# Kernel tuning notes

Measured on AMD Instinct MI355X. Metric: run time of the kernel, lower is better.

Reference implementation:

```python
import jax, jax.numpy as jnp
import numpy as np

B, M, E, IN, Q, OUT, H = 256, 2048, 128, 512, 512, 512, 64

def _lin(x, w, b):
    return x @ w.T + b

def setup_inputs() -> dict:
    key = jax.random.key(0)
    ks = jax.random.split(key, 20)
    d = {
        'read_weights': jax.random.uniform(ks[0], (B, M)),
        'write_weights': jax.random.uniform(ks[1], (B, M)),
        'usage': jax.random.uniform(ks[2], (B, M)),
        'free_gates': jax.random.uniform(ks[3], (B, M)),
        'x': jax.random.normal(ks[4], (B, 1, IN)),
        'query': jax.random.normal(ks[5], (B, 1, Q)),
        'memory': jax.random.normal(ks[6], (B, M, E)),
        'I_w': jax.random.normal(ks[7], (E, IN)) * 0.02, 'I_b': jnp.zeros((E,)),
        'W1_w': jax.random.normal(ks[8], (H, E)) * 0.02, 'W1_b': jnp.zeros((H,)),
        'W2_w': jax.random.normal(ks[9], (H, E)) * 0.02, 'W2_b': jnp.zeros((H,)),
        'R1_w': jax.random.normal(ks[10], (H, Q)) * 0.02, 'R1_b': jnp.zeros((H,)),
        'R2_w': jax.random.normal(ks[11], (H, E)) * 0.02, 'R2_b': jnp.zeros((H,)),
        'O_w': jax.random.normal(ks[12], (OUT, E)) * 0.02, 'O_b': jnp.zeros((OUT,)),
    }
    return d

def _allocation(read_weights, write_weights, usage, free_gates):
    u = 1e-5 + (1.0 - 1e-5) * usage
    psi = 1.0 - free_gates * read_weights
    u = u + write_weights - u * write_weights
    u = u * psi                                   # new usage [B, M]
    phi = jnp.argsort(u, axis=1)                  # ascending order indices
    sorted_u = jnp.take_along_axis(u, phi, axis=1)
    # NOTE: original uses inclusive cumprod (matches torch code exactly)
    sorted_alloc = (1.0 - sorted_u) * jnp.cumprod(sorted_u, axis=1)
    phi_rev = jnp.argsort(phi, axis=1)            # inverse permutation
    alloc = jnp.take_along_axis(sorted_alloc, phi_rev, axis=1)
    return u, alloc

def reference(read_weights, write_weights, usage, free_gates, x, query, memory,
              I_w, I_b, W1_w, W1_b, W2_w, W2_b, R1_w, R1_b, R2_w, R2_b, O_w, O_b):
    # ---- write ----
    emb = _lin(x, I_w, I_b)                       # [B,1,E]
    Wi = _lin(emb, W1_w, W1_b)                    # [B,1,H]
    Wm = _lin(memory, W2_w, W2_b)                 # [B,M,H]
    scores = jnp.einsum('bqh,bmh->bqm', Wi, Wm)   # [B,1,M]
    w_content = jax.nn.softmax(scores, axis=2)
    new_usage, alloc = _allocation(read_weights, write_weights, usage, free_gates)
    w = (w_content + alloc[:, None, :]) * 0.5     # [B,1,M]
    new_memory = memory + w.transpose(0, 2, 1) * emb  # [B,M,1]*[B,1,E]
    new_write_weights = w[:, 0, :]
    # ---- read ----
    Rq = _lin(query, R1_w, R1_b)                  # [B,1,H]
    Rm = _lin(new_memory, R2_w, R2_b)             # [B,M,H]
    rscores = jnp.einsum('bqh,bmh->bqm', Rq, Rm)
    wr = jax.nn.softmax(rscores, axis=2)          # [B,1,M]
    pooled = jnp.einsum('bm,bme->be', wr[:, 0, :], new_memory)
    output = _lin(pooled, O_w, O_b)               # [B,OUT]
    return ((wr[:, 0, :], new_write_weights, new_usage), output, new_memory)
```

## Files before the change

### kernel.cpp

```cpp
#include <hip/hip_runtime.h>
#include <hip/hip_bf16.h>

constexpr int B   = 256;
constexpr int M   = 2048;
constexpr int E   = 128;
constexpr int IN  = 512;
constexpr int Qd  = 512;
constexpr int OUTd= 512;
constexpr int H   = 64;

constexpr size_t OFF_WR = 0;
constexpr size_t OFF_W  = (size_t)B*M;
constexpr size_t OFF_U  = (size_t)2*B*M;
constexpr size_t OFF_Y  = (size_t)3*B*M;
constexpr size_t OFF_NM = OFF_Y + (size_t)B*OUTd;

__device__ __forceinline__ float bf2f(unsigned short u) {
    union { unsigned int i; float f; } v; v.i = ((unsigned int)u) << 16; return v.f;
}
__device__ __forceinline__ unsigned short f2bf(float f) {
    unsigned int x = __float_as_uint(f);
    unsigned int r = (x + 0x7fffu + ((x >> 16) & 1u)) >> 16;
    return (unsigned short)r;
}
__device__ __forceinline__ void unpack8(uint4 d, float* o) {
    o[0]=bf2f(d.x & 0xffff); o[1]=bf2f(d.x >> 16);
    o[2]=bf2f(d.y & 0xffff); o[3]=bf2f(d.y >> 16);
    o[4]=bf2f(d.z & 0xffff); o[5]=bf2f(d.z >> 16);
    o[6]=bf2f(d.w & 0xffff); o[7]=bf2f(d.w >> 16);
}
__device__ __forceinline__ uint4 pack8(const float* f) {
    uint4 d;
    d.x = (unsigned)f2bf(f[0]) | ((unsigned)f2bf(f[1]) << 16);
    d.y = (unsigned)f2bf(f[2]) | ((unsigned)f2bf(f[3]) << 16);
    d.z = (unsigned)f2bf(f[4]) | ((unsigned)f2bf(f[5]) << 16);
    d.w = (unsigned)f2bf(f[6]) | ((unsigned)f2bf(f[7]) << 16);
    return d;
}

__device__ __forceinline__ float ldf(const void* p, size_t i, int bf) {
    return bf ? bf2f(((const unsigned short*)p)[i]) : ((const float*)p)[i];
}
__device__ __forceinline__ void ld8(const void* p, size_t i, int bf, float* o) {
    if (bf) {
        uint4 d = *(const uint4*)((const unsigned short*)p + i);
        unpack8(d, o);
    } else {
        const float4* q = (const float4*)((const float*)p + i);
        float4 a = q[0], c = q[1];
        o[0]=a.x; o[1]=a.y; o[2]=a.z; o[3]=a.w;
        o[4]=c.x; o[5]=c.y; o[6]=c.z; o[7]=c.w;
    }
}
__device__ __forceinline__ void st1(void* p, size_t i, int bf, float v) {
    if (bf) ((unsigned short*)p)[i] = f2bf(v);
    else    ((float*)p)[i] = v;
}
__device__ __forceinline__ void st8(void* p, size_t i, int bf, const float* v) {
    if (bf) {
        *(uint4*)((unsigned short*)p + i) = pack8(v);
    } else {
        float4 a, c;
        a.x=v[0]; a.y=v[1]; a.z=v[2]; a.w=v[3];
        c.x=v[4]; c.y=v[5]; c.z=v[6]; c.w=v[7];
        float4* q = (float4*)((float*)p + i);
        q[0]=a; q[1]=c;
    }
}

__global__ __launch_bounds__(512) void k0_detect(const void* usage, int* flag) {
    __shared__ int cnt;
    if (threadIdx.x == 0) cnt = 0;
    __syncthreads();
    float v = bf2f(((const unsigned short*)usage)[threadIdx.x]);
    int ok = (v >= 0.0f && v <= 1.0f) ? 1 : 0;
    atomicAdd(&cnt, ok);
    __syncthreads();
    if (threadIdx.x == 0) flag[0] = (cnt >= 500) ? 1 : 0;
}

__global__ __launch_bounds__(128) void k1_pre(
    const void* __restrict__ x,   const void* __restrict__ qy,
    const void* __restrict__ I_w, const void* __restrict__ I_b,
    const void* __restrict__ W1w, const void* __restrict__ W1b,
    const void* __restrict__ W2w, const void* __restrict__ W2b,
    const void* __restrict__ R1w, const void* __restrict__ R1b,
    const void* __restrict__ R2w, const void* __restrict__ R2b,
    const int* __restrict__ flag,
    float* __restrict__ emb_ws, float* __restrict__ v_ws, float* __restrict__ u2_ws,
    float* __restrict__ c1_ws,  float* __restrict__ c2_ws, float* __restrict__ d2_ws)
{
    const int bf = *flag;
    __shared__ float xs[IN], qs[Qd], embs[E], wis[H], rqs[H], red[128];
    const int b = blockIdx.x, t = threadIdx.x;

    for (int i = t; i < IN; i += 128) xs[i] = ldf(x,  (size_t)b*IN + i, bf);
    for (int i = t; i < Qd; i += 128) qs[i] = ldf(qy, (size_t)b*Qd + i, bf);
    __syncthreads();

    float acc = 0.f;
    for (int c = 0; c < IN/8; ++c) {
        float m8[8]; ld8(I_w, (size_t)t*IN + c*8, bf, m8);
        #pragma unroll
        for (int j = 0; j < 8; ++j) acc += m8[j] * xs[c*8 + j];
    }
    acc += ldf(I_b, t, bf);
    embs[t] = acc;
    emb_ws[(size_t)b*E + t] = acc;
    __syncthreads();

    if (t < H) {
        float wv = 0.f;
        for (int c = 0; c < E/8; ++c) {
            float m8[8]; ld8(W1w, (size_t)t*E + c*8, bf, m8);
            #pragma unroll
            for (int j = 0; j < 8; ++j) wv += m8[j] * embs[c*8 + j];
        }
        wv += ldf(W1b, t, bf);
        wis[t] = wv;
    }
    __syncthreads();

    float vv = 0.f;
    for (int h = 0; h < H; ++h) vv += ldf(W2w, (size_t)h*E + t, bf) * wis[h];
    v_ws[(size_t)b*E + t] = vv;

    red[t] = (t < H) ? wis[t] * ldf(W2b, t, bf) : 0.f;
    __syncthreads();
    for (int off = 64; off > 0; off >>= 1) { if (t < off) red[t] += red[t+off]; __syncthreads(); }
    if (t == 0) c1_ws[b] = red[0];
    __syncthreads();

    if (t < H) {
        float rv = 0.f;
        for (int c = 0; c < Qd/8; ++c) {
            float m8[8]; ld8(R1w, (size_t)t*Qd + c*8, bf, m8);
            #pragma unroll
            for (int j = 0; j < 8; ++j) rv += m8[j] * qs[c*8 + j];
        }
        rv += ldf(R1b, t, bf);
        rqs[t] = rv;
    }
    __syncthreads();

    float uu = 0.f;
    for (int h = 0; h < H; ++h) uu += ldf(R2w, (size_t)h*E + t, bf) * rqs[h];
    u2_ws[(size_t)b*E + t] = uu;

    red[t] = (t < H) ? rqs[t] * ldf(R2b, t, bf) : 0.f;
    __syncthreads();
    for (int off = 64; off > 0; off >>= 1) { if (t < off) red[t] += red[t+off]; __syncthreads(); }
    if (t == 0) c2_ws[b] = red[0];
    __syncthreads();

    red[t] = uu * embs[t];
    __syncthreads();
    for (int off = 64; off > 0; off >>= 1) { if (t < off) red[t] += red[t+off]; __syncthreads(); }
    if (t == 0) d2_ws[b] = red[0];
}

__global__ __launch_bounds__(256) void k2_alloc(
    const void* __restrict__ rw, const void* __restrict__ ww,
    const void* __restrict__ us, const void* __restrict__ fg,
    const int* __restrict__ flag,
    float* __restrict__ alloc_ws, void* __restrict__ dout)
{
    const int bf = *flag;
    __shared__ float uv[M];
    __shared__ int   idx[M];
    __shared__ float scan[256];
    const int b = blockIdx.x, t = threadIdx.x;

    #pragma unroll
    for (int s = 0; s < 8; ++s) {
        int m = s*256 + t;
        size_t o = (size_t)b*M + m;
        float U = ldf(us, o, bf), W = ldf(ww, o, bf), R = ldf(rw, o, bf), F = ldf(fg, o, bf);
        float u = 1e-5f + (1.0f - 1e-5f) * U;
        float psi = 1.0f - F * R;
        u = u + W - u * W;
        u = u * psi;
        uv[m] = u; idx[m] = m;
        st1(dout, OFF_U + o, bf, u);
    }
    __syncthreads();

    for (int k = 2; k <= M; k <<= 1) {
        for (int j = k >> 1; j > 0; j >>= 1) {
            #pragma unroll
            for (int s = 0; s < 8; ++s) {
                int i = s*256 + t;
                int ixj = i ^ j;
                if (ixj > i) {
                    bool up = ((i & k) == 0);
                    float a = uv[i], c = uv[ixj];
                    int ia = idx[i], ic = idx[ixj];
                    bool agtb = (a > c) || (a == c && ia > ic);
                    if (up ? agtb : !agtb) {
                        uv[i] = c; uv[ixj] = a;
                        idx[i] = ic; idx[ixj] = ia;
                    }
                }
            }
            __syncthreads();
        }
    }

    const int base = t * 8;
    float lp[8];
    float run = 1.f;
    #pragma unroll
    for (int q = 0; q < 8; ++q) { run *= uv[base + q]; lp[q] = run; }
    scan[t] = run;
    __syncthreads();
    for (int off = 1; off < 256; off <<= 1) {
        float val = scan[t];
        float oth = (t >= off) ? scan[t - off] : 1.0f;
        __syncthreads();
        scan[t] = val * oth;
        __syncthreads();
    }
    float pref = (t > 0) ? scan[t - 1] : 1.0f;

    #pragma unroll
    for (int q = 0; q < 8; ++q) {
        int i = base + q;
        float a = (1.0f - uv[i]) * (pref * lp[q]);
        alloc_ws[(size_t)b*M + idx[i]] = a;
    }
}

__global__ __launch_bounds__(256) void k3_scores(
    const void* __restrict__ mem,
    const float* __restrict__ v_ws, const float* __restrict__ u2_ws,
    const float* __restrict__ c1_ws, const int* __restrict__ flag,
    float* __restrict__ s1, float* __restrict__ s2)
{
    const int bf = *flag;
    const int blk = blockIdx.x;
    const int b = blk >> 4, chunk = blk & 15;
    const int t = threadIdx.x, l = t & 15, g = t >> 4;
    float v8[8], u8[8];
    {
        const float* vb = v_ws  + (size_t)b*E + l*8;
        const float* ub = u2_ws + (size_t)b*E + l*8;
        #pragma unroll
        for (int j = 0; j < 8; ++j) { v8[j] = vb[j]; u8[j] = ub[j]; }
    }
    const float cc1 = c1_ws[b];
    const size_t mbase = (size_t)b*M*E;
    const int row0 = chunk*128 + g;
    for (int it = 0; it < 8; ++it) {
        int row = row0 + it*16;
        float m8[8]; ld8(mem, mbase + (size_t)row*E + l*8, bf, m8);
        float p1 = 0.f, p2 = 0.f;
        #pragma unroll
        for (int j = 0; j < 8; ++j) { p1 += m8[j]*v8[j]; p2 += m8[j]*u8[j]; }
        #pragma unroll
        for (int mask = 8; mask > 0; mask >>= 1) {
            p1 += __shfl_xor(p1, mask, 16);
            p2 += __shfl_xor(p2, mask, 16);
        }
        if (l == 0) {
            s1[(size_t)b*M + row] = p1 + cc1;
            s2[(size_t)b*M + row] = p2;
        }
    }
}

__global__ __launch_bounds__(256) void k4_weights(
    const float* __restrict__ s1, const float* __restrict__ s2,
    const float* __restrict__ alloc_ws,
    const float* __restrict__ c2_ws, const float* __restrict__ d2_ws,
    const int* __restrict__ flag,
    float* __restrict__ w_ws, float* __restrict__ wr_ws,
    void* __restrict__ dout)
{
    const int bf = *flag;
    __shared__ float red[256];
    const int b = blockIdx.x, t = threadIdx.x;
    const float* s1b = s1 + (size_t)b*M;
    const float* s2b = s2 + (size_t)b*M;

    float sv[8];
    float lmax = -3.4e38f;
    #pragma unroll
    for (int s = 0; s < 8; ++s) { sv[s] = s1b[s*256 + t]; lmax = fmaxf(lmax, sv[s]); }
    red[t] = lmax; __syncthreads();
    for (int off = 128; off > 0; off >>= 1) { if (t < off) red[t] = fmaxf(red[t], red[t+off]); __syncthreads(); }
    float gmax = red[0]; __syncthreads();

    float lsum = 0.f;
    #pragma unroll
    for (int s = 0; s < 8; ++s) { float e = expf(sv[s] - gmax); sv[s] = e; lsum += e; }
    red[t] = lsum; __syncthreads();
    for (int off = 128; off > 0; off >>= 1) { if (t < off) red[t] += red[t+off]; __syncthreads(); }
    float inv = 1.0f / red[0]; __syncthreads();

    const float dd = d2_ws[b], cc = c2_ws[b];
    float rs[8];
    #pragma unroll
    for (int s = 0; s < 8; ++s) {
        int m = s*256 + t;
        float wc = sv[s] * inv;
        float wv = 0.5f * (wc + alloc_ws[(size_t)b*M + m]);
        w_ws[(size_t)b*M + m] = wv;
        st1(dout, OFF_W + (size_t)b*M + m, bf, wv);
        rs[s] = s2b[m] + wv * dd + cc;
    }

    lmax = -3.4e38f;
    #pragma unroll
    for (int s = 0; s < 8; ++s) lmax = fmaxf(lmax, rs[s]);
    red[t] = lmax; __syncthreads();
    for (int off = 128; off > 0; off >>= 1) { if (t < off) red[t] = fmaxf(red[t], red[t+off]); __syncthreads(); }
    gmax = red[0]; __syncthreads();

    lsum = 0.f;
    #pragma unroll
    for (int s = 0; s < 8; ++s) { float e = expf(rs[s] - gmax); rs[s] = e; lsum += e; }
    red[t] = lsum; __syncthreads();
    for (int off = 128; off > 0; off >>= 1) { if (t < off) red[t] += red[t+off]; __syncthreads(); }
    float inv2 = 1.0f / red[0]; __syncthreads();

    #pragma unroll
    for (int s = 0; s < 8; ++s) {
        int m = s*256 + t;
        float wrv = rs[s] * inv2;
        wr_ws[(size_t)b*M + m] = wrv;
        st1(dout, OFF_WR + (size_t)b*M + m, bf, wrv);
    }
}

__global__ __launch_bounds__(256) void k5_update(
    const void* __restrict__ mem, const float* __restrict__ emb_ws,
    const float* __restrict__ w_ws, const float* __restrict__ wr_ws,
    const int* __restrict__ flag,
    void* __restrict__ dout, float* __restrict__ pooled)
{
    const int bf = *flag;
    __shared__ float psh[E];
    const int blk = blockIdx.x;
    const int b = blk >> 4, chunk = blk & 15;
    const int t = threadIdx.x, l = t & 15, g = t >> 4;
    if (t < E) psh[t] = 0.f;
    __syncthreads();

    float e8[8];
    {
        const float* eb = emb_ws + (size_t)b*E + l*8;
        #pragma unroll
        for (int j = 0; j < 8; ++j) e8[j] = eb[j];
    }
    float acc[8] = {0,0,0,0,0,0,0,0};
    const size_t mbase = (size_t)b*M*E;
    const int row0 = chunk*128 + g;
    for (int it = 0; it < 8; ++it) {
        int row = row0 + it*16;
        size_t off = mbase + (size_t)row*E + l*8;
        float m8[8]; ld8(mem, off, bf, m8);
        float wv  = w_ws [(size_t)b*M + row];
        float wrv = wr_ws[(size_t)b*M + row];
        float n8[8];
        #pragma unroll
        for (int j = 0; j < 8; ++j) {
            n8[j] = m8[j] + wv * e8[j];
            acc[j] += wrv * n8[j];
        }
        st8(dout, OFF_NM + off, bf, n8);
    }
    #pragma unroll
    for (int j = 0; j < 8; ++j) atomicAdd(&psh[l*8 + j], acc[j]);
    __syncthreads();
    if (t < E) atomicAdd(&pooled[(size_t)b*E + t], psh[t]);
}

__global__ __launch_bounds__(256) void k6_out(
    const float* __restrict__ pooled,
    const void* __restrict__ O_w, const void* __restrict__ O_b,
    const int* __restrict__ flag,
    void* __restrict__ dout)
{
    const int bf = *flag;
    __shared__ float ps[E];
    const int b = blockIdx.x, t = threadIdx.x;
    if (t < E) ps[t] = pooled[(size_t)b*E + t];
    __syncthreads();
    for (int o = t; o < OUTd; o += 256) {
        float acc = 0.f;
        for (int c = 0; c < E/8; ++c) {
            float m8[8]; ld8(O_w, (size_t)o*E + c*8, bf, m8);
            #pragma unroll
            for (int j = 0; j < 8; ++j) acc += m8[j] * ps[c*8 + j];
        }
        acc += ldf(O_b, o, bf);
        st1(dout, OFF_Y + (size_t)b*OUTd + o, bf, acc);
    }
}

extern "C" void kernel_launch(void* const* d_in, const int* in_sizes, int n_in,
                              void* d_out, int out_size, void* d_ws, size_t ws_size,
                              hipStream_t stream)
{
    const void* rw  = d_in[0];
    const void* ww  = d_in[1];
    const void* us  = d_in[2];
    const void* fg  = d_in[3];
    const void* x   = d_in[4];
    const void* qy  = d_in[5];
    const void* mem = d_in[6];
    const void* I_w = d_in[7];
    const void* I_b = d_in[8];
    const void* W1w = d_in[9];
    const void* W1b = d_in[10];
    const void* W2w = d_in[11];
    const void* W2b = d_in[12];
    const void* R1w = d_in[13];
    const void* R1b = d_in[14];
    const void* R2w = d_in[15];
    const void* R2b = d_in[16];
    const void* O_w = d_in[17];
    const void* O_b = d_in[18];

    int*   flag_ws = (int*)d_ws;
    float* fbase   = (float*)d_ws + 16;
    float* emb_ws   = fbase;
    float* v_ws     = emb_ws + (size_t)B*E;
    float* u2_ws    = v_ws   + (size_t)B*E;
    float* c1_ws    = u2_ws  + (size_t)B*E;
    float* c2_ws    = c1_ws  + B;
    float* d2_ws    = c2_ws  + B;
    float* alloc_ws = d2_ws  + B;
    float* s1_ws    = alloc_ws + (size_t)B*M;
    float* s2_ws    = s1_ws    + (size_t)B*M;
    float* w_ws     = s2_ws    + (size_t)B*M;
    float* wr_ws    = w_ws     + (size_t)B*M;
    float* pooled   = wr_ws    + (size_t)B*M;

    hipMemsetAsync(pooled, 0, (size_t)B*E*sizeof(float), stream);

    k0_detect<<<1,    512, 0, stream>>>(us, flag_ws);
    k1_pre   <<<B,    128, 0, stream>>>(x, qy, I_w, I_b, W1w, W1b, W2w, W2b,
                                        R1w, R1b, R2w, R2b, flag_ws,
                                        emb_ws, v_ws, u2_ws, c1_ws, c2_ws, d2_ws);
    k2_alloc <<<B,    256, 0, stream>>>(rw, ww, us, fg, flag_ws, alloc_ws, d_out);
    k3_scores<<<B*16, 256, 0, stream>>>(mem, v_ws, u2_ws, c1_ws, flag_ws, s1_ws, s2_ws);
    k4_weights<<<B,   256, 0, stream>>>(s1_ws, s2_ws, alloc_ws, c2_ws, d2_ws, flag_ws,
                                        w_ws, wr_ws, d_out);
    k5_update<<<B*16, 256, 0, stream>>>(mem, emb_ws, w_ws, wr_ws, flag_ws, d_out, pooled);
    k6_out   <<<B,    256, 0, stream>>>(pooled, O_w, O_b, flag_ws, d_out);
}
```

Before: 714.5 us.

## Fuse alloc sort with score kernel, register bitonic sort, deterministic pooled partials

```diff
diff --git a/kernel.cpp b/kernel.cpp
--- a/kernel.cpp
+++ b/kernel.cpp
@@ -79,7 +79,7 @@
     if (threadIdx.x == 0) flag[0] = (cnt >= 500) ? 1 : 0;
 }
 
-__global__ __launch_bounds__(128) void k1_pre(
+__global__ __launch_bounds__(256) void k1_pre(
     const void* __restrict__ x,   const void* __restrict__ qy,
     const void* __restrict__ I_w, const void* __restrict__ I_b,
     const void* __restrict__ W1w, const void* __restrict__ W1b,
@@ -88,25 +88,39 @@
     const void* __restrict__ R2w, const void* __restrict__ R2b,
     const int* __restrict__ flag,
     float* __restrict__ emb_ws, float* __restrict__ v_ws, float* __restrict__ u2_ws,
-    float* __restrict__ c1_ws,  float* __restrict__ c2_ws, float* __restrict__ d2_ws)
+    float* __restrict__ c1_ws,  float* __restrict__ c2_ws)
 {
     const int bf = *flag;
-    __shared__ float xs[IN], qs[Qd], embs[E], wis[H], rqs[H], red[128];
+    __shared__ float xs[IN], qs[Qd], embs[E], wis[H], rqs[H], red[256];
     const int b = blockIdx.x, t = threadIdx.x;
 
-    for (int i = t; i < IN; i += 128) xs[i] = ldf(x,  (size_t)b*IN + i, bf);
-    for (int i = t; i < Qd; i += 128) qs[i] = ldf(qy, (size_t)b*Qd + i, bf);
-    __syncthreads();
-
-    float acc = 0.f;
-    for (int c = 0; c < IN/8; ++c) {
-        float m8[8]; ld8(I_w, (size_t)t*IN + c*8, bf, m8);
-        #pragma unroll
-        for (int j = 0; j < 8; ++j) acc += m8[j] * xs[c*8 + j];
-    }
-    acc += ldf(I_b, t, bf);
-    embs[t] = acc;
-    emb_ws[(size_t)b*E + t] = acc;
+    for (int i = t; i < IN; i += 256) xs[i] = ldf(x,  (size_t)b*IN + i, bf);
+    for (int i = t; i < Qd; i += 256) qs[i] = ldf(qy, (size_t)b*Qd + i, bf);
+    __syncthreads();
+
+    if (t < 128) {
+        float acc = 0.f;
+        for (int c = 0; c < IN/8; ++c) {
+            float m8[8]; ld8(I_w, (size_t)t*IN + c*8, bf, m8);
+            #pragma unroll
+            for (int j = 0; j < 8; ++j) acc += m8[j] * xs[c*8 + j];
+        }
+        acc += ldf(I_b, t, bf);
+        embs[t] = acc;
+        emb_ws[(size_t)b*E + t] = acc;
+    } else {
+        int t2 = t - 128;
+        if (t2 < H) {
+            float rv = 0.f;
+            for (int c = 0; c < Qd/8; ++c) {
+                float m8[8]; ld8(R1w, (size_t)t2*Qd + c*8, bf, m8);
+                #pragma unroll
+                for (int j = 0; j < 8; ++j) rv += m8[j] * qs[c*8 + j];
+            }
+            rv += ldf(R1b, t2, bf);
+            rqs[t2] = rv;
+        }
+    }
     __syncthreads();
 
     if (t < H) {
@@ -118,152 +132,162 @@
         }
         wv += ldf(W1b, t, bf);
         wis[t] = wv;
-    }
-    __syncthreads();
-
-    float vv = 0.f;
-    for (int h = 0; h < H; ++h) vv += ldf(W2w, (size_t)h*E + t, bf) * wis[h];
-    v_ws[(size_t)b*E + t] = vv;
-
-    red[t] = (t < H) ? wis[t] * ldf(W2b, t, bf) : 0.f;
-    __syncthreads();
-    for (int off = 64; off > 0; off >>= 1) { if (t < off) red[t] += red[t+off]; __syncthreads(); }
-    if (t == 0) c1_ws[b] = red[0];
-    __syncthreads();
-
-    if (t < H) {
-        float rv = 0.f;
-        for (int c = 0; c < Qd/8; ++c) {
-            float m8[8]; ld8(R1w, (size_t)t*Qd + c*8, bf, m8);
-            #pragma unroll
-            for (int j = 0; j < 8; ++j) rv += m8[j] * qs[c*8 + j];
-        }
-        rv += ldf(R1b, t, bf);
-        rqs[t] = rv;
-    }
-    __syncthreads();
-
-    float uu = 0.f;
-    for (int h = 0; h < H; ++h) uu += ldf(R2w, (size_t)h*E + t, bf) * rqs[h];
-    u2_ws[(size_t)b*E + t] = uu;
-
-    red[t] = (t < H) ? rqs[t] * ldf(R2b, t, bf) : 0.f;
-    __syncthreads();
-    for (int off = 64; off > 0; off >>= 1) { if (t < off) red[t] += red[t+off]; __syncthreads(); }
-    if (t == 0) c2_ws[b] = red[0];
-    __syncthreads();
-
-    red[t] = uu * embs[t];
-    __syncthreads();
-    for (int off = 64; off > 0; off >>= 1) { if (t < off) red[t] += red[t+off]; __syncthreads(); }
-    if (t == 0) d2_ws[b] = red[0];
-}
-
-__global__ __launch_bounds__(256) void k2_alloc(
+    } else if (t >= 128) {
+        int t2 = t - 128;
+        float uu = 0.f;
+        for (int h = 0; h < H; ++h) uu += ldf(R2w, (size_t)h*E + t2, bf) * rqs[h];
+        u2_ws[(size_t)b*E + t2] = uu;
+        red[t] = (t2 < H) ? rqs[t2] * ldf(R2b, t2, bf) : 0.f;
+    }
+    __syncthreads();
+
+    if (t < 128) {
+        float vv = 0.f;
+        for (int h = 0; h < H; ++h) vv += ldf(W2w, (size_t)h*E + t, bf) * wis[h];
+        v_ws[(size_t)b*E + t] = vv;
+        red[t] = (t < H) ? wis[t] * ldf(W2b, t, bf) : 0.f;
+    }
+    __syncthreads();
+
+    for (int off = 64; off > 0; off >>= 1) {
+        if (t < off) red[t] += red[t + off];
+        if (t >= 128 && t < 128 + off) red[t] += red[t + off];
+        __syncthreads();
+    }
+    if (t == 0)   c1_ws[b] = red[0];
+    if (t == 128) c2_ws[b] = red[128];
+}
+
+__global__ __launch_bounds__(256) void kB_alloc_scores(
     const void* __restrict__ rw, const void* __restrict__ ww,
     const void* __restrict__ us, const void* __restrict__ fg,
-    const int* __restrict__ flag,
-    float* __restrict__ alloc_ws, void* __restrict__ dout)
-{
+    const void* __restrict__ mem,
+    const float* __restrict__ v_ws, const float* __restrict__ u2_ws,
+    const float* __restrict__ c1_ws, const int* __restrict__ flag,
+    float* __restrict__ alloc_ws, float* __restrict__ s1, float* __restrict__ s2,
+    void* __restrict__ dout)
+{
+    __shared__ unsigned long long sh64[M];
+    __shared__ float scan[256];
     const int bf = *flag;
-    __shared__ float uv[M];
-    __shared__ int   idx[M];
-    __shared__ float scan[256];
-    const int b = blockIdx.x, t = threadIdx.x;
-
-    #pragma unroll
-    for (int s = 0; s < 8; ++s) {
-        int m = s*256 + t;
-        size_t o = (size_t)b*M + m;
-        float U = ldf(us, o, bf), W = ldf(ww, o, bf), R = ldf(rw, o, bf), F = ldf(fg, o, bf);
-        float u = 1e-5f + (1.0f - 1e-5f) * U;
-        float psi = 1.0f - F * R;
-        u = u + W - u * W;
-        u = u * psi;
-        uv[m] = u; idx[m] = m;
-        st1(dout, OFF_U + o, bf, u);
-    }
-    __syncthreads();
-
-    for (int k = 2; k <= M; k <<= 1) {
-        for (int j = k >> 1; j > 0; j >>= 1) {
-            #pragma unroll
-            for (int s = 0; s < 8; ++s) {
-                int i = s*256 + t;
-                int ixj = i ^ j;
-                if (ixj > i) {
-                    bool up = ((i & k) == 0);
-                    float a = uv[i], c = uv[ixj];
-                    int ia = idx[i], ic = idx[ixj];
-                    bool agtb = (a > c) || (a == c && ia > ic);
-                    if (up ? agtb : !agtb) {
-                        uv[i] = c; uv[ixj] = a;
-                        idx[i] = ic; idx[ixj] = ia;
+    const int t = threadIdx.x;
+
+    if (blockIdx.x < B) {
+        const int b = blockIdx.x;
+        const size_t base = (size_t)b*M + (size_t)t*8;
+        float r8[8], w8[8], u8[8], f8[8], nu[8];
+        ld8(rw, base, bf, r8); ld8(ww, base, bf, w8);
+        ld8(us, base, bf, u8); ld8(fg, base, bf, f8);
+
+        unsigned long long key[8];
+        #pragma unroll
+        for (int q = 0; q < 8; ++q) {
+            float u = 1e-5f + (1.0f - 1e-5f) * u8[q];
+            float psi = 1.0f - f8[q] * r8[q];
+            u = u + w8[q] - u * w8[q];
+            u = u * psi;
+            nu[q] = u;
+            unsigned fb = __float_as_uint(u);
+            fb = (fb & 0x80000000u) ? ~fb : (fb | 0x80000000u);
+            key[q] = ((unsigned long long)fb << 32) | (unsigned)(t*8 + q);
+        }
+        st8(dout, OFF_U + base, bf, nu);
+
+        for (int k = 2; k <= M; k <<= 1) {
+            for (int j = k >> 1; j > 0; j >>= 1) {
+                if (j >= 512) {
+                    __syncthreads();
+                    #pragma unroll
+                    for (int q = 0; q < 8; ++q) sh64[t*8 + q] = key[q];
+                    __syncthreads();
+                    const bool up      = (((t << 3) & k) == 0);
+                    const bool lower   = (((t << 3) & j) == 0);
+                    const bool keepmin = (lower == up);
+                    #pragma unroll
+                    for (int q = 0; q < 8; ++q) {
+                        unsigned long long o = sh64[(t*8 + q) ^ j];
+                        bool take = keepmin ? (o < key[q]) : (o > key[q]);
+                        if (take) key[q] = o;
+                    }
+                } else if (j >= 8) {
+                    const int d = j >> 3;
+                    const bool up      = (((t << 3) & k) == 0);
+                    const bool keepmin = (((t & d) == 0) == up);
+                    #pragma unroll
+                    for (int q = 0; q < 8; ++q) {
+                        unsigned long long o = __shfl_xor(key[q], d, 64);
+                        bool take = keepmin ? (o < key[q]) : (o > key[q]);
+                        if (take) key[q] = o;
+                    }
+                } else {
+                    #pragma unroll
+                    for (int q = 0; q < 8; ++q) {
+                        if (!(q & j)) {
+                            int p = q | j;
+                            bool up = ((((t << 3) + q) & k) == 0);
+                            unsigned long long a = key[q], c = key[p];
+                            bool sw = up ? (a > c) : (a < c);
+                            if (sw) { key[q] = c; key[p] = a; }
+                        }
                     }
                 }
             }
+        }
+
+        float su[8], lp[8]; int sidx[8];
+        #pragma unroll
+        for (int q = 0; q < 8; ++q) {
+            unsigned fb = (unsigned)(key[q] >> 32);
+            fb = (fb & 0x80000000u) ? (fb ^ 0x80000000u) : ~fb;
+            su[q]   = __uint_as_float(fb);
+            sidx[q] = (int)(key[q] & 0xffffffffu);
+        }
+        float run = 1.f;
+        #pragma unroll
+        for (int q = 0; q < 8; ++q) { run *= su[q]; lp[q] = run; }
+        scan[t] = run;
+        __syncthreads();
+        for (int off = 1; off < 256; off <<= 1) {
+            float val = scan[t];
+            float oth = (t >= off) ? scan[t - off] : 1.0f;
             __syncthreads();
-        }
-    }
-
-    const int base = t * 8;
-    float lp[8];
-    float run = 1.f;
-    #pragma unroll
-    for (int q = 0; q < 8; ++q) { run *= uv[base + q]; lp[q] = run; }
-    scan[t] = run;
-    __syncthreads();
-    for (int off = 1; off < 256; off <<= 1) {
-        float val = scan[t];
-        float oth = (t >= off) ? scan[t - off] : 1.0f;
-        __syncthreads();
-        scan[t] = val * oth;
-        __syncthreads();
-    }
-    float pref = (t > 0) ? scan[t - 1] : 1.0f;
-
-    #pragma unroll
-    for (int q = 0; q < 8; ++q) {
-        int i = base + q;
-        float a = (1.0f - uv[i]) * (pref * lp[q]);
-        alloc_ws[(size_t)b*M + idx[i]] = a;
-    }
-}
-
-__global__ __launch_bounds__(256) void k3_scores(
-    const void* __restrict__ mem,
-    const float* __restrict__ v_ws, const float* __restrict__ u2_ws,
-    const float* __restrict__ c1_ws, const int* __restrict__ flag,
-    float* __restrict__ s1, float* __restrict__ s2)
-{
-    const int bf = *flag;
-    const int blk = blockIdx.x;
-    const int b = blk >> 4, chunk = blk & 15;
-    const int t = threadIdx.x, l = t & 15, g = t >> 4;
-    float v8[8], u8[8];
-    {
-        const float* vb = v_ws  + (size_t)b*E + l*8;
-        const float* ub = u2_ws + (size_t)b*E + l*8;
-        #pragma unroll
-        for (int j = 0; j < 8; ++j) { v8[j] = vb[j]; u8[j] = ub[j]; }
-    }
-    const float cc1 = c1_ws[b];
-    const size_t mbase = (size_t)b*M*E;
-    const int row0 = chunk*128 + g;
-    for (int it = 0; it < 8; ++it) {
-        int row = row0 + it*16;
-        float m8[8]; ld8(mem, mbase + (size_t)row*E + l*8, bf, m8);
-        float p1 = 0.f, p2 = 0.f;
-        #pragma unroll
-        for (int j = 0; j < 8; ++j) { p1 += m8[j]*v8[j]; p2 += m8[j]*u8[j]; }
-        #pragma unroll
-        for (int mask = 8; mask > 0; mask >>= 1) {
-            p1 += __shfl_xor(p1, mask, 16);
-            p2 += __shfl_xor(p2, mask, 16);
-        }
-        if (l == 0) {
-            s1[(size_t)b*M + row] = p1 + cc1;
-            s2[(size_t)b*M + row] = p2;
+            scan[t] = val * oth;
+            __syncthreads();
+        }
+        float pref = (t > 0) ? scan[t - 1] : 1.0f;
+        #pragma unroll
+        for (int q = 0; q < 8; ++q)
+            alloc_ws[(size_t)b*M + sidx[q]] = (1.0f - su[q]) * (pref * lp[q]);
+
+    } else {
+        const int blk = blockIdx.x - B;
+        const int b = blk >> 4, chunk = blk & 15;
+        const int l = t & 15, g = t >> 4;
+        float v8[8], u8[8];
+        {
+            const float* vb = v_ws  + (size_t)b*E + l*8;
+            const float* ub = u2_ws + (size_t)b*E + l*8;
+            #pragma unroll
+            for (int j = 0; j < 8; ++j) { v8[j] = vb[j]; u8[j] = ub[j]; }
+        }
+        const float cc1 = c1_ws[b];
+        const size_t mbase = (size_t)b*M*E;
+        const int row0 = chunk*128 + g;
+        for (int it = 0; it < 8; ++it) {
+            int row = row0 + it*16;
+            float m8[8]; ld8(mem, mbase + (size_t)row*E + l*8, bf, m8);
+            float p1 = 0.f, p2 = 0.f;
+            #pragma unroll
+            for (int j = 0; j < 8; ++j) { p1 += m8[j]*v8[j]; p2 += m8[j]*u8[j]; }
+            #pragma unroll
+            for (int mask = 8; mask > 0; mask >>= 1) {
+                p1 += __shfl_xor(p1, mask, 16);
+                p2 += __shfl_xor(p2, mask, 16);
+            }
+            if (l == 0) {
+                s1[(size_t)b*M + row] = p1 + cc1;
+                s2[(size_t)b*M + row] = p2;
+            }
         }
     }
 }
@@ -271,7 +295,8 @@
 __global__ __launch_bounds__(256) void k4_weights(
     const float* __restrict__ s1, const float* __restrict__ s2,
     const float* __restrict__ alloc_ws,
-    const float* __restrict__ c2_ws, const float* __restrict__ d2_ws,
+    const float* __restrict__ c2_ws,
+    const float* __restrict__ u2_ws, const float* __restrict__ emb_ws,
     const int* __restrict__ flag,
     float* __restrict__ w_ws, float* __restrict__ wr_ws,
     void* __restrict__ dout)
@@ -282,6 +307,13 @@
     const float* s1b = s1 + (size_t)b*M;
     const float* s2b = s2 + (size_t)b*M;
 
+    red[t] = (t < E) ? u2_ws[(size_t)b*E + t] * emb_ws[(size_t)b*E + t] : 0.f;
+    __syncthreads();
+    for (int off = 128; off > 0; off >>= 1) { if (t < off) red[t] += red[t+off]; __syncthreads(); }
+    const float dd = red[0];
+    const float cc = c2_ws[b];
+    __syncthreads();
+
     float sv[8];
     float lmax = -3.4e38f;
     #pragma unroll
@@ -297,7 +329,6 @@
     for (int off = 128; off > 0; off >>= 1) { if (t < off) red[t] += red[t+off]; __syncthreads(); }
     float inv = 1.0f / red[0]; __syncthreads();
 
-    const float dd = d2_ws[b], cc = c2_ws[b];
     float rs[8];
     #pragma unroll
     for (int s = 0; s < 8; ++s) {
@@ -336,15 +367,13 @@
     const void* __restrict__ mem, const float* __restrict__ emb_ws,
     const float* __restrict__ w_ws, const float* __restrict__ wr_ws,
     const int* __restrict__ flag,
-    void* __restrict__ dout, float* __restrict__ pooled)
+    void* __restrict__ dout, float* __restrict__ pooled_p)
 {
     const int bf = *flag;
-    __shared__ float psh[E];
+    __shared__ float pw[4][E];
     const int blk = blockIdx.x;
     const int b = blk >> 4, chunk = blk & 15;
     const int t = threadIdx.x, l = t & 15, g = t >> 4;
-    if (t < E) psh[t] = 0.f;
-    __syncthreads();
 
     float e8[8];
     {
@@ -370,13 +399,23 @@
         st8(dout, OFF_NM + off, bf, n8);
     }
     #pragma unroll
-    for (int j = 0; j < 8; ++j) atomicAdd(&psh[l*8 + j], acc[j]);
-    __syncthreads();
-    if (t < E) atomicAdd(&pooled[(size_t)b*E + t], psh[t]);
+    for (int j = 0; j < 8; ++j) {
+        acc[j] += __shfl_xor(acc[j], 16, 64);
+        acc[j] += __shfl_xor(acc[j], 32, 64);
+    }
+    const int wid = t >> 6;
+    if ((t & 63) < 16) {
+        const int l0 = t & 15;
+        #pragma unroll
+        for (int j = 0; j < 8; ++j) pw[wid][l0*8 + j] = acc[j];
+    }
+    __syncthreads();
+    if (t < E)
+        pooled_p[((size_t)b*16 + chunk)*E + t] = pw[0][t] + pw[1][t] + pw[2][t] + pw[3][t];
 }
 
 __global__ __launch_bounds__(256) void k6_out(
-    const float* __restrict__ pooled,
+    const float* __restrict__ pooled_p,
     const void* __restrict__ O_w, const void* __restrict__ O_b,
     const int* __restrict__ flag,
     void* __restrict__ dout)
@@ -384,7 +423,12 @@
     const int bf = *flag;
     __shared__ float ps[E];
     const int b = blockIdx.x, t = threadIdx.x;
-    if (t < E) ps[t] = pooled[(size_t)b*E + t];
+    if (t < E) {
+        float s = 0.f;
+        #pragma unroll
+        for (int c = 0; c < 16; ++c) s += pooled_p[((size_t)b*16 + c)*E + t];
+        ps[t] = s;
+    }
     __syncthreads();
     for (int o = t; o < OUTd; o += 256) {
         float acc = 0.f;
@@ -429,24 +473,24 @@
     float* u2_ws    = v_ws   + (size_t)B*E;
     float* c1_ws    = u2_ws  + (size_t)B*E;
     float* c2_ws    = c1_ws  + B;
-    float* d2_ws    = c2_ws  + B;
-    float* alloc_ws = d2_ws  + B;
+    float* alloc_ws = c2_ws  + B;
     float* s1_ws    = alloc_ws + (size_t)B*M;
     float* s2_ws    = s1_ws    + (size_t)B*M;
     float* w_ws     = s2_ws    + (size_t)B*M;
     float* wr_ws    = w_ws     + (size_t)B*M;
-    float* pooled   = wr_ws    + (size_t)B*M;
-
-    hipMemsetAsync(pooled, 0, (size_t)B*E*sizeof(float), stream);
-
-    k0_detect<<<1,    512, 0, stream>>>(us, flag_ws);
-    k1_pre   <<<B,    128, 0, stream>>>(x, qy, I_w, I_b, W1w, W1b, W2w, W2b,
-                                        R1w, R1b, R2w, R2b, flag_ws,
-                                        emb_ws, v_ws, u2_ws, c1_ws, c2_ws, d2_ws);
-    k2_alloc <<<B,    256, 0, stream>>>(rw, ww, us, fg, flag_ws, alloc_ws, d_out);
-    k3_scores<<<B*16, 256, 0, stream>>>(mem, v_ws, u2_ws, c1_ws, flag_ws, s1_ws, s2_ws);
-    k4_weights<<<B,   256, 0, stream>>>(s1_ws, s2_ws, alloc_ws, c2_ws, d2_ws, flag_ws,
-                                        w_ws, wr_ws, d_out);
-    k5_update<<<B*16, 256, 0, stream>>>(mem, emb_ws, w_ws, wr_ws, flag_ws, d_out, pooled);
-    k6_out   <<<B,    256, 0, stream>>>(pooled, O_w, O_b, flag_ws, d_out);
-}
+    float* pooled_p = alloc_ws;
+
+    k0_detect<<<1,        512, 0, stream>>>(us, flag_ws);
+    k1_pre   <<<B,        256, 0, stream>>>(x, qy, I_w, I_b, W1w, W1b, W2w, W2b,
+                                            R1w, R1b, R2w, R2b, flag_ws,
+                                            emb_ws, v_ws, u2_ws, c1_ws, c2_ws);
+    kB_alloc_scores<<<B + B*16, 256, 0, stream>>>(rw, ww, us, fg, mem,
+                                            v_ws, u2_ws, c1_ws, flag_ws,
+                                            alloc_ws, s1_ws, s2_ws, d_out);
+    k4_weights<<<B,       256, 0, stream>>>(s1_ws, s2_ws, alloc_ws, c2_ws,
+                                            u2_ws, emb_ws, flag_ws,
+                                            w_ws, wr_ws, d_out);
+    k5_update<<<B*16,     256, 0, stream>>>(mem, emb_ws, w_ws, wr_ws, flag_ws,
+                                            d_out, pooled_p);
+    k6_out   <<<B,        256, 0, stream>>>(pooled_p, O_w, O_b, flag_ws, d_out);
+}
```

Result: faster. 616.8 us (-13.7%).
